# Performance work log

Hardware: AMD Instinct MI355X
Metric: run time of the kernel (lower is better)

Reference implementation:

```python
import jax, jax.numpy as jnp
import numpy as np

TEMPERATURE = 0.5
NORMALIZE = True


def setup_inputs() -> dict:
    key = jax.random.key(0)
    k1, k2 = jax.random.split(key)
    B, D = 4096, 256
    z1 = jax.random.normal(k1, (B, D), dtype=jnp.float32)
    z2 = jax.random.normal(k2, (B, D), dtype=jnp.float32)
    return {"z1": z1, "z2": z2}


def reference(z1, z2):
    B = z1.shape[0]
    if NORMALIZE:
        z1 = z1 / jnp.linalg.norm(z1, axis=1, keepdims=True)
        z2 = z2 / jnp.linalg.norm(z2, axis=1, keepdims=True)
    z = jnp.concatenate([z1, z2], axis=0)          # [2B, D]
    sim = (z @ z.T) / TEMPERATURE                   # [2B, 2B]
    n = 2 * B
    idx = jnp.arange(n)
    pos_idx = (idx + B) % n                         # positive pair index per row
    pos = sim[idx, pos_idx]                         # [2B] positive logits
    # mask self-similarity (diagonal); positives stay in denominator (cross_entropy
    # denominator = pos + all negatives, which equals all non-diagonal entries)
    neg_inf = jnp.finfo(sim.dtype).min
    masked = jnp.where(idx[:, None] == idx[None, :], neg_inf, sim)
    lse = jax.scipy.special.logsumexp(masked, axis=1)  # [2B]
    loss = jnp.mean(lse - pos)
    return loss
```

## Files before the change

### kernel.cpp

```cpp
#include <hip/hip_runtime.h>
#include <hip/hip_bf16.h>

#define B_ROWS 4096
#define D_DIM  256
#define N_ROWS 8192
#define NT     64
#define NTRI   (NT * (NT + 1) / 2)

typedef __attribute__((ext_vector_type(8))) __bf16 bf16x8;
typedef __attribute__((ext_vector_type(4))) float  f32x4;

#if defined(__has_builtin)
#if __has_builtin(__builtin_amdgcn_exp2f)
#define EXP2(x) __builtin_amdgcn_exp2f(x)
#else
#define EXP2(x) exp2f(x)
#endif
#else
#define EXP2(x) exp2f(x)
#endif

static __device__ __forceinline__ float wave_reduce_add(float v) {
#pragma unroll
    for (int m = 32; m >= 1; m >>= 1) v += __shfl_xor(v, m, 64);
    return v;
}

static __device__ __forceinline__ unsigned short f2bf(float f) {
    __hip_bfloat16 h = __float2bfloat16(f);
    return __builtin_bit_cast(unsigned short, h);
}

__global__ __launch_bounds__(256) void norm_pos_kernel(
    const float* __restrict__ z1, const float* __restrict__ z2,
    unsigned short* __restrict__ zb, float* __restrict__ pos,
    float* __restrict__ rowsum, float* __restrict__ out)
{
    const int w = threadIdx.x >> 6, l = threadIdx.x & 63;
    const int i = blockIdx.x * 4 + w;

    const float4 a = *reinterpret_cast<const float4*>(z1 + (size_t)i * D_DIM + l * 4);
    const float4 b = *reinterpret_cast<const float4*>(z2 + (size_t)i * D_DIM + l * 4);

    float ss1 = a.x * a.x + a.y * a.y + a.z * a.z + a.w * a.w;
    float ss2 = b.x * b.x + b.y * b.y + b.z * b.z + b.w * b.w;
    float dp  = a.x * b.x + a.y * b.y + a.z * b.z + a.w * b.w;
    ss1 = wave_reduce_add(ss1);
    ss2 = wave_reduce_add(ss2);
    dp  = wave_reduce_add(dp);

    const float inv1 = rsqrtf(ss1);
    const float inv2 = rsqrtf(ss2);
    if (l == 0) pos[i] = 2.0f * dp * inv1 * inv2;

    ushort4 ua, ub;
    ua.x = f2bf(a.x * inv1); ua.y = f2bf(a.y * inv1);
    ua.z = f2bf(a.z * inv1); ua.w = f2bf(a.w * inv1);
    ub.x = f2bf(b.x * inv2); ub.y = f2bf(b.y * inv2);
    ub.z = f2bf(b.z * inv2); ub.w = f2bf(b.w * inv2);

    reinterpret_cast<ushort4*>(zb + (size_t)i * D_DIM)[l] = ua;
    reinterpret_cast<ushort4*>(zb + (size_t)(i + B_ROWS) * D_DIM)[l] = ub;

    if (threadIdx.x < 8) rowsum[blockIdx.x * 8 + threadIdx.x] = 0.0f;
    if (blockIdx.x == 0 && threadIdx.x == 0) *out = 0.0f;
}

__global__ __launch_bounds__(256) void simsum_kernel(
    const unsigned short* __restrict__ zb, float* __restrict__ rowsum)
{
    const int idx = blockIdx.x;
    int by = (int)((2.0f * NT + 1.0f -
                    sqrtf((2.0f * NT + 1.0f) * (2.0f * NT + 1.0f) - 8.0f * idx)) * 0.5f);
    if (by < 0) by = 0;
    if (by > NT - 1) by = NT - 1;
#define TRI_START(b) ((b) * NT - (((b) * ((b) - 1)) >> 1))
    while (TRI_START(by) > idx) --by;
    while (by < NT - 1 && TRI_START(by + 1) <= idx) ++by;
    const int bx = by + (idx - TRI_START(by));
#undef TRI_START

    const int brow = by * 128, bcol = bx * 128;
    const bool isdiag = (bx == by);
    const int tid = threadIdx.x;
    const int w = tid >> 6, l = tid & 63;
    const int wr = w >> 1, wc = w & 1;
    const int g = l >> 4, c15 = l & 15;

    __shared__ __align__(16) unsigned short Atile[128 * 64];
    __shared__ __align__(16) unsigned short Btile[128 * 64];
    __shared__ float rowbuf[2][128];
    __shared__ float colbuf[2][128];

    f32x4 acc[4][4];
#pragma unroll
    for (int mi = 0; mi < 4; ++mi)
#pragma unroll
        for (int ni = 0; ni < 4; ++ni) acc[mi][ni] = (f32x4){0.f, 0.f, 0.f, 0.f};

#pragma unroll
    for (int ks = 0; ks < 4; ++ks) {
        const int k0 = ks * 64;
#pragma unroll
        for (int it = 0; it < 4; ++it) {
            const int c = it * 256 + tid;
            const int row = c >> 3;
            const int cpos = c & 7;
            const int kc = (cpos ^ (row & 7)) * 8;
            const unsigned short* srcA = zb + (size_t)(brow + row) * D_DIM + k0 + kc;
            const unsigned short* srcB = zb + (size_t)(bcol + row) * D_DIM + k0 + kc;
            __builtin_amdgcn_global_load_lds(
                (const __attribute__((address_space(1))) void*)srcA,
                (__attribute__((address_space(3))) void*)(Atile + c * 8), 16, 0, 0);
            __builtin_amdgcn_global_load_lds(
                (const __attribute__((address_space(1))) void*)srcB,
                (__attribute__((address_space(3))) void*)(Btile + c * 8), 16, 0, 0);
        }
        __syncthreads();

#pragma unroll
        for (int s = 0; s < 2; ++s) {
            bf16x8 a[4], b[4];
#pragma unroll
            for (int mi = 0; mi < 4; ++mi) {
                const int row = wr * 64 + mi * 16 + c15;
                a[mi] = *reinterpret_cast<const bf16x8*>(
                    Atile + row * 64 + (((s * 4 + g) ^ (row & 7)) * 8));
            }
#pragma unroll
            for (int ni = 0; ni < 4; ++ni) {
                const int row = wc * 64 + ni * 16 + c15;
                b[ni] = *reinterpret_cast<const bf16x8*>(
                    Btile + row * 64 + (((s * 4 + g) ^ (row & 7)) * 8));
            }
#pragma unroll
            for (int mi = 0; mi < 4; ++mi)
#pragma unroll
                for (int ni = 0; ni < 4; ++ni)
                    acc[mi][ni] = __builtin_amdgcn_mfma_f32_16x16x32_bf16(
                        a[mi], b[ni], acc[mi][ni], 0, 0, 0);
        }
        __syncthreads();
    }

    float colacc[4] = {0.f, 0.f, 0.f, 0.f};
#pragma unroll
    for (int mi = 0; mi < 4; ++mi) {
        f32x4 rs = {0.f, 0.f, 0.f, 0.f};
#pragma unroll
        for (int ni = 0; ni < 4; ++ni) {
            const int gcol = bcol + wc * 64 + ni * 16 + c15;
#pragma unroll
            for (int r = 0; r < 4; ++r) {
                const int grow = brow + wr * 64 + mi * 16 + g * 4 + r;
                float e = EXP2(acc[mi][ni][r] * 2.8853900817779268f);
                if (isdiag && grow == gcol) e = 0.f;
                rs[r] += e;
                colacc[ni] += e;
            }
        }
#pragma unroll
        for (int m = 1; m < 16; m <<= 1)
#pragma unroll
            for (int r = 0; r < 4; ++r) rs[r] += __shfl_xor(rs[r], m, 64);
        if (c15 == 0)
#pragma unroll
            for (int r = 0; r < 4; ++r)
                rowbuf[wc][wr * 64 + mi * 16 + g * 4 + r] = rs[r];
    }
#pragma unroll
    for (int ni = 0; ni < 4; ++ni) {
        colacc[ni] += __shfl_xor(colacc[ni], 16, 64);
        colacc[ni] += __shfl_xor(colacc[ni], 32, 64);
    }
    if (l < 16)
#pragma unroll
        for (int ni = 0; ni < 4; ++ni)
            colbuf[wr][wc * 64 + ni * 16 + c15] = colacc[ni];
    __syncthreads();

    if (tid < 128) {
        atomicAdd(&rowsum[brow + tid], rowbuf[0][tid] + rowbuf[1][tid]);
        if (!isdiag)
            atomicAdd(&rowsum[bcol + tid], colbuf[0][tid] + colbuf[1][tid]);
    }
}

__global__ __launch_bounds__(256) void reduce_kernel(
    const float* __restrict__ rowsum, const float* __restrict__ pos,
    float* __restrict__ out)
{
    const int r = blockIdx.x * 256 + threadIdx.x;
    float val = logf(rowsum[r]) - pos[r & (B_ROWS - 1)];

    val = wave_reduce_add(val);
    __shared__ float red[4];
    if ((threadIdx.x & 63) == 0) red[threadIdx.x >> 6] = val;
    __syncthreads();
    if (threadIdx.x == 0)
        atomicAdd(out, (red[0] + red[1] + red[2] + red[3]) * (1.0f / 8192.0f));
}

extern "C" void kernel_launch(void* const* d_in, const int* in_sizes, int n_in,
                              void* d_out, int out_size, void* d_ws, size_t ws_size,
                              hipStream_t stream)
{
    const float* z1 = (const float*)d_in[0];
    const float* z2 = (const float*)d_in[1];
    float* out = (float*)d_out;

    char* ws = (char*)d_ws;
    unsigned short* zb = (unsigned short*)ws;
    float* pos         = (float*)(ws + 4u * 1024 * 1024);
    float* rowsum      = (float*)(ws + 4u * 1024 * 1024 + 64 * 1024);

    hipLaunchKernelGGL(norm_pos_kernel, dim3(B_ROWS / 4), dim3(256), 0, stream,
                       z1, z2, zb, pos, rowsum, out);
    hipLaunchKernelGGL(simsum_kernel, dim3(NTRI), dim3(256), 0, stream,
                       zb, rowsum);
    hipLaunchKernelGGL(reduce_kernel, dim3(N_ROWS / 256), dim3(256), 0, stream,
                       rowsum, pos, out);
}
```

Baseline: 90.43 us.

## Double-buffer LDS k-tiles and fold final reduction into last simsum block

```diff
diff --git a/kernel.cpp b/kernel.cpp
--- a/kernel.cpp
+++ b/kernel.cpp
@@ -34,7 +34,7 @@
 __global__ __launch_bounds__(256) void norm_pos_kernel(
     const float* __restrict__ z1, const float* __restrict__ z2,
     unsigned short* __restrict__ zb, float* __restrict__ pos,
-    float* __restrict__ rowsum, float* __restrict__ out)
+    float* __restrict__ rowsum, int* __restrict__ cnt)
 {
     const int w = threadIdx.x >> 6, l = threadIdx.x & 63;
     const int i = blockIdx.x * 4 + w;
@@ -63,11 +63,13 @@
     reinterpret_cast<ushort4*>(zb + (size_t)(i + B_ROWS) * D_DIM)[l] = ub;
 
     if (threadIdx.x < 8) rowsum[blockIdx.x * 8 + threadIdx.x] = 0.0f;
-    if (blockIdx.x == 0 && threadIdx.x == 0) *out = 0.0f;
+    if (blockIdx.x == 0 && threadIdx.x == 0) *cnt = 0;
 }
 
 __global__ __launch_bounds__(256) void simsum_kernel(
-    const unsigned short* __restrict__ zb, float* __restrict__ rowsum)
+    const unsigned short* __restrict__ zb, float* __restrict__ rowsum,
+    const float* __restrict__ pos, int* __restrict__ cnt,
+    float* __restrict__ out)
 {
     const int idx = blockIdx.x;
     int by = (int)((2.0f * NT + 1.0f -
@@ -87,8 +89,8 @@
     const int wr = w >> 1, wc = w & 1;
     const int g = l >> 4, c15 = l & 15;
 
-    __shared__ __align__(16) unsigned short Atile[128 * 64];
-    __shared__ __align__(16) unsigned short Btile[128 * 64];
+    __shared__ __align__(16) unsigned short Atile[2][128 * 64];
+    __shared__ __align__(16) unsigned short Btile[2][128 * 64];
     __shared__ float rowbuf[2][128];
     __shared__ float colbuf[2][128];
 
@@ -98,9 +100,7 @@
 #pragma unroll
         for (int ni = 0; ni < 4; ++ni) acc[mi][ni] = (f32x4){0.f, 0.f, 0.f, 0.f};
 
-#pragma unroll
-    for (int ks = 0; ks < 4; ++ks) {
-        const int k0 = ks * 64;
+    auto STAGE = [&](int buf, int k0) {
 #pragma unroll
         for (int it = 0; it < 4; ++it) {
             const int c = it * 256 + tid;
@@ -111,13 +111,14 @@
             const unsigned short* srcB = zb + (size_t)(bcol + row) * D_DIM + k0 + kc;
             __builtin_amdgcn_global_load_lds(
                 (const __attribute__((address_space(1))) void*)srcA,
-                (__attribute__((address_space(3))) void*)(Atile + c * 8), 16, 0, 0);
+                (__attribute__((address_space(3))) void*)(&Atile[buf][c * 8]), 16, 0, 0);
             __builtin_amdgcn_global_load_lds(
                 (const __attribute__((address_space(1))) void*)srcB,
-                (__attribute__((address_space(3))) void*)(Btile + c * 8), 16, 0, 0);
-        }
-        __syncthreads();
-
+                (__attribute__((address_space(3))) void*)(&Btile[buf][c * 8]), 16, 0, 0);
+        }
+    };
+
+    auto COMPUTE = [&](int buf) {
 #pragma unroll
         for (int s = 0; s < 2; ++s) {
             bf16x8 a[4], b[4];
@@ -125,13 +126,13 @@
             for (int mi = 0; mi < 4; ++mi) {
                 const int row = wr * 64 + mi * 16 + c15;
                 a[mi] = *reinterpret_cast<const bf16x8*>(
-                    Atile + row * 64 + (((s * 4 + g) ^ (row & 7)) * 8));
+                    &Atile[buf][row * 64 + (((s * 4 + g) ^ (row & 7)) * 8)]);
             }
 #pragma unroll
             for (int ni = 0; ni < 4; ++ni) {
                 const int row = wc * 64 + ni * 16 + c15;
                 b[ni] = *reinterpret_cast<const bf16x8*>(
-                    Btile + row * 64 + (((s * 4 + g) ^ (row & 7)) * 8));
+                    &Btile[buf][row * 64 + (((s * 4 + g) ^ (row & 7)) * 8)]);
             }
 #pragma unroll
             for (int mi = 0; mi < 4; ++mi)
@@ -140,8 +141,17 @@
                     acc[mi][ni] = __builtin_amdgcn_mfma_f32_16x16x32_bf16(
                         a[mi], b[ni], acc[mi][ni], 0, 0, 0);
         }
+    };
+
+    STAGE(0, 0);
+    __syncthreads();
+#pragma unroll
+    for (int ks = 0; ks < 3; ++ks) {
+        STAGE((ks + 1) & 1, (ks + 1) * 64);
+        COMPUTE(ks & 1);
         __syncthreads();
     }
+    COMPUTE(1);
 
     float colacc[4] = {0.f, 0.f, 0.f, 0.f};
 #pragma unroll
@@ -184,21 +194,24 @@
         if (!isdiag)
             atomicAdd(&rowsum[bcol + tid], colbuf[0][tid] + colbuf[1][tid]);
     }
-}
-
-__global__ __launch_bounds__(256) void reduce_kernel(
-    const float* __restrict__ rowsum, const float* __restrict__ pos,
-    float* __restrict__ out)
-{
-    const int r = blockIdx.x * 256 + threadIdx.x;
-    float val = logf(rowsum[r]) - pos[r & (B_ROWS - 1)];
-
-    val = wave_reduce_add(val);
-    __shared__ float red[4];
-    if ((threadIdx.x & 63) == 0) red[threadIdx.x >> 6] = val;
+
+    __threadfence();
+    __shared__ int lastflag;
+    if (tid == 0) lastflag = (atomicAdd(cnt, 1) == NTRI - 1);
     __syncthreads();
-    if (threadIdx.x == 0)
-        atomicAdd(out, (red[0] + red[1] + red[2] + red[3]) * (1.0f / 8192.0f));
+    if (lastflag) {
+        float part = 0.0f;
+        for (int r = tid; r < N_ROWS; r += 256) {
+            const float s = atomicAdd(&rowsum[r], 0.0f);
+            part += logf(s) - pos[r & (B_ROWS - 1)];
+        }
+        part = wave_reduce_add(part);
+        __shared__ float red[4];
+        if ((tid & 63) == 0) red[tid >> 6] = part;
+        __syncthreads();
+        if (tid == 0)
+            *out = (red[0] + red[1] + red[2] + red[3]) * (1.0f / 8192.0f);
+    }
 }
 
 extern "C" void kernel_launch(void* const* d_in, const int* in_sizes, int n_in,
@@ -213,11 +226,10 @@
     unsigned short* zb = (unsigned short*)ws;
     float* pos         = (float*)(ws + 4u * 1024 * 1024);
     float* rowsum      = (float*)(ws + 4u * 1024 * 1024 + 64 * 1024);
+    int*   cnt         = (int*)  (ws + 4u * 1024 * 1024 + 128 * 1024);
 
     hipLaunchKernelGGL(norm_pos_kernel, dim3(B_ROWS / 4), dim3(256), 0, stream,
-                       z1, z2, zb, pos, rowsum, out);
+                       z1, z2, zb, pos, rowsum, cnt);
     hipLaunchKernelGGL(simsum_kernel, dim3(NTRI), dim3(256), 0, stream,
-                       zb, rowsum);
-    hipLaunchKernelGGL(reduce_kernel, dim3(N_ROWS / 256), dim3(256), 0, stream,
-                       rowsum, pos, out);
-}
+                       zb, rowsum, pos, cnt, out);
+}
```

Result: slower. 216.6 us (+139.5%).
